# Optimization experiments

Measured on AMD Instinct MI355X. Metric: run time of the kernel, lower is better.

The kernel has to match this reference:

```python
import jax, jax.numpy as jnp
import numpy as np

EPS_DEFAULT = 1.1920928955078125e-07  # torch fp32 finfo eps used when eps=None


def rms_norm(x, ndims, weight=None, eps=EPS_DEFAULT):
    # normalize over the last `ndims` dims, matching F.rms_norm semantics
    axes = tuple(range(x.ndim - ndims, x.ndim))
    ms = jnp.mean(jnp.square(x), axis=axes, keepdims=True)
    out = x * jax.lax.rsqrt(ms + eps)
    if weight is not None:
        out = out * weight  # weight broadcasts over trailing dims
    return out


def setup_inputs() -> dict:
    key = jax.random.key(0)
    ks = jax.random.split(key, 9)
    B, S = 32, 512
    return {
        "x": jax.random.normal(ks[0], (B, S, 12, 24), dtype=jnp.float32),
        "y": jax.random.normal(ks[1], (B, S, 12, 16), dtype=jnp.float32),
        "z": jax.random.normal(ks[2], (B, S, 12, 16, 24), dtype=jnp.float32),
        "w0": jax.random.uniform(ks[3], (24,), dtype=jnp.float32),
        "w1": jax.random.uniform(ks[4], (12, 16), dtype=jnp.float32),
        "w2": jax.random.uniform(ks[5], (24,), dtype=jnp.float32),
        "w3": jax.random.uniform(ks[6], (24,), dtype=jnp.float32),
        "w4": jax.random.uniform(ks[7], (12, 16), dtype=jnp.float32),
        "w5": jax.random.uniform(ks[8], (24,), dtype=jnp.float32),
    }


def reference(x, y, z, w0, w1, w2, w3, w4, w5):
    # x branch: norm over (24,), then (12,24), then (24,)
    x = rms_norm(x, 1, w0)
    x = rms_norm(x, 2, None)
    x = rms_norm(x, 1, w3)
    # y branch: norm over (16,) eps=1e-3, then (12,16) twice
    y = rms_norm(y, 1, None, eps=0.001)
    y = rms_norm(y, 2, w1)
    y = rms_norm(y, 2, w4)
    # z branch: norm over (24,), then (12,16,24) eps=1e-2, then (24,)
    z = rms_norm(z, 1, w2)
    z = rms_norm(z, 3, None, eps=0.01)
    z = rms_norm(z, 1, w5)
    return (x, y, z)
```

## Files before the change

kernel.cpp:

```cpp
#include <hip/hip_runtime.h>

#define EPS_DEF 1.1920928955078125e-07f


__launch_bounds__(256)
__global__ void fused_rms_kernel(const float* __restrict__ x,
                                 const float* __restrict__ y,
                                 const float* __restrict__ z,
                                 const float* __restrict__ w0,
                                 const float* __restrict__ w1,
                                 const float* __restrict__ w2,
                                 const float* __restrict__ w3,
                                 const float* __restrict__ w4,
                                 const float* __restrict__ w5,
                                 float* __restrict__ ox,
                                 float* __restrict__ oy,
                                 float* __restrict__ oz)
{
    __shared__ float zs[192 * 25];
    __shared__ float xs[12 * 25];
    __shared__ float ys[12 * 17];
    __shared__ float w0s[24], w2s[24], w3s[24], w5s[24];
    __shared__ float w1s[192], w4s[192];
    __shared__ float wpart[4][4];
    __shared__ float az[192], ax[12], ay[12];

    const int tid = threadIdx.x;
    const int bid = blockIdx.x;

    if (tid < 24) {
        w0s[tid] = w0[tid];
        w2s[tid] = w2[tid];
        w3s[tid] = w3[tid];
        w5s[tid] = w5[tid];
    }
    if (tid < 192) {
        w1s[tid] = w1[tid];
        w4s[tid] = w4[tid];
    }

    const float4* zp = (const float4*)(z + (size_t)bid * 4608);
    const float4* xp = (const float4*)(x + (size_t)bid * 288);
    const float4* yp = (const float4*)(y + (size_t)bid * 192);

    for (int v = tid; v < 1152; v += 256) {
        float4 q = zp[v];
        int k = v * 4, r = k / 24, c = k - r * 24;
        float* d = &zs[r * 25 + c];
        d[0] = q.x; d[1] = q.y; d[2] = q.z; d[3] = q.w;
    }
    if (tid < 72) {
        float4 q = xp[tid];
        int k = tid * 4, r = k / 24, c = k - r * 24;
        float* d = &xs[r * 25 + c];
        d[0] = q.x; d[1] = q.y; d[2] = q.z; d[3] = q.w;
    }
    if (tid < 48) {
        float4 q = yp[tid];
        int k = tid * 4, r = k / 16, c = k - r * 16;
        float* d = &ys[r * 17 + c];
        d[0] = q.x; d[1] = q.y; d[2] = q.z; d[3] = q.w;
    }
    __syncthreads();

    float p0 = 0.f, p1 = 0.f, p2 = 0.f, p3 = 0.f;
    float r1 = 0.f, sw = 0.f;

    if (tid < 192) {
        const float* row = &zs[tid * 25];
        float s0 = 0.f, s = 0.f;
        #pragma unroll
        for (int j = 0; j < 24; ++j) {
            float v = row[j];
            float vw = v * w2s[j];
            s0 += v * v;
            s += vw * vw;
        }
        r1 = rsqrtf(s0 * (1.f / 24.f) + EPS_DEF);
        sw = s;
        p0 = r1 * r1 * s;
    } else if (tid < 204) {
        int i = tid - 192;
        const float* row = &xs[i * 25];
        float s0 = 0.f, s = 0.f;
        #pragma unroll
        for (int j = 0; j < 24; ++j) {
            float v = row[j];
            float vw = v * w0s[j];
            s0 += v * v;
            s += vw * vw;
        }
        r1 = rsqrtf(s0 * (1.f / 24.f) + EPS_DEF);
        sw = s;
        p1 = r1 * r1 * s;
    } else if (tid < 216) {
        int i = tid - 204;
        const float* row = &ys[i * 17];
        const float* w1r = &w1s[i * 16];
        float s0 = 0.f, s = 0.f;
        #pragma unroll
        for (int j = 0; j < 16; ++j) {
            float v = row[j];
            float vw = v * w1r[j];
            s0 += v * v;
            s += vw * vw;
        }
        r1 = rsqrtf(s0 * (1.f / 16.f) + 1e-3f);
        sw = s;
        p2 = r1 * r1 * s0;
        p3 = r1 * r1 * s;
    }

    #pragma unroll
    for (int d = 32; d > 0; d >>= 1) {
        p0 += __shfl_down(p0, d, 64);
        p1 += __shfl_down(p1, d, 64);
        p2 += __shfl_down(p2, d, 64);
        p3 += __shfl_down(p3, d, 64);
    }
    const int wave = tid >> 6;
    if ((tid & 63) == 0) {
        wpart[wave][0] = p0; wpart[wave][1] = p1;
        wpart[wave][2] = p2; wpart[wave][3] = p3;
    }
    __syncthreads();

    const float Sz  = wpart[0][0] + wpart[1][0] + wpart[2][0] + wpart[3][0];
    const float Sx  = wpart[0][1] + wpart[1][1] + wpart[2][1] + wpart[3][1];
    const float Sy0 = wpart[0][2] + wpart[1][2] + wpart[2][2] + wpart[3][2];
    const float Sy1 = wpart[0][3] + wpart[1][3] + wpart[2][3] + wpart[3][3];

    const float cZ  = rsqrtf(Sz  * (1.f / 4608.f) + 0.01f);
    const float cX  = rsqrtf(Sx  * (1.f / 288.f)  + EPS_DEF);
    const float c2y = rsqrtf(Sy0 * (1.f / 192.f)  + EPS_DEF);
    const float c3y = rsqrtf(c2y * c2y * Sy1 * (1.f / 192.f) + EPS_DEF);

    if (tid < 192) {
        float r3 = rsqrtf(cZ * cZ * r1 * r1 * sw * (1.f / 24.f) + EPS_DEF);
        az[tid] = r1 * cZ * r3;
    } else if (tid < 204) {
        float r3 = rsqrtf(cX * cX * r1 * r1 * sw * (1.f / 24.f) + EPS_DEF);
        ax[tid - 192] = r1 * cX * r3;
    } else if (tid < 216) {
        ay[tid - 204] = r1 * c2y * c3y;
    }
    __syncthreads();

    float4* ozp = (float4*)(oz + (size_t)bid * 4608);
    for (int v = tid; v < 1152; v += 256) {
        int k = v * 4, r = k / 24, c = k - r * 24;
        const float* s = &zs[r * 25 + c];
        float a = az[r];
        float4 q;
        q.x = s[0] * a * w2s[c + 0] * w5s[c + 0];
        q.y = s[1] * a * w2s[c + 1] * w5s[c + 1];
        q.z = s[2] * a * w2s[c + 2] * w5s[c + 2];
        q.w = s[3] * a * w2s[c + 3] * w5s[c + 3];
        ozp[v] = q;
    }
    if (tid < 72) {
        int k = tid * 4, r = k / 24, c = k - r * 24;
        const float* s = &xs[r * 25 + c];
        float a = ax[r];
        float4 q;
        q.x = s[0] * a * w0s[c + 0] * w3s[c + 0];
        q.y = s[1] * a * w0s[c + 1] * w3s[c + 1];
        q.z = s[2] * a * w0s[c + 2] * w3s[c + 2];
        q.w = s[3] * a * w0s[c + 3] * w3s[c + 3];
        ((float4*)(ox + (size_t)bid * 288))[tid] = q;
    }
    if (tid < 48) {
        int k = tid * 4, r = k / 16, c = k - r * 16;
        const float* s = &ys[r * 17 + c];
        float a = ay[r];
        float4 q;
        q.x = s[0] * a * w1s[k + 0] * w4s[k + 0];
        q.y = s[1] * a * w1s[k + 1] * w4s[k + 1];
        q.z = s[2] * a * w1s[k + 2] * w4s[k + 2];
        q.w = s[3] * a * w1s[k + 3] * w4s[k + 3];
        ((float4*)(oy + (size_t)bid * 192))[tid] = q;
    }
}

extern "C" void kernel_launch(void* const* d_in, const int* in_sizes, int n_in,
                              void* d_out, int out_size, void* d_ws, size_t ws_size,
                              hipStream_t stream) {
    const float* x  = (const float*)d_in[0];
    const float* y  = (const float*)d_in[1];
    const float* z  = (const float*)d_in[2];
    const float* w0 = (const float*)d_in[3];
    const float* w1 = (const float*)d_in[4];
    const float* w2 = (const float*)d_in[5];
    const float* w3 = (const float*)d_in[6];
    const float* w4 = (const float*)d_in[7];
    const float* w5 = (const float*)d_in[8];

    float* out = (float*)d_out;
    const size_t NX = (size_t)32 * 512 * 12 * 24;
    const size_t NY = (size_t)32 * 512 * 12 * 16;
    float* ox = out;
    float* oy = out + NX;
    float* oz = out + NX + NY;

    const int nblk = 32 * 512;
    hipLaunchKernelGGL(fused_rms_kernel, dim3(nblk), dim3(256), 0, stream,
                       x, y, z, w0, w1, w2, w3, w4, w5, ox, oy, oz);
}
```

Measured before the change: 139.1 us.

## Keep z rows in registers per thread and precompute squared and combined weights

Each of 192 threads now loads one 24-element z row straight into registers, so z no longer goes through LDS and the az broadcast array plus one barrier are dropped. The weights are precombined once per block into squared and product forms, which saves multiplies. Block size falls from 256 to 192, and x/y row outputs are written per row. In exchange, each thread's global accesses are strided by 96 bytes, so loads and stores are less coalesced per instruction, and register pressure rises from holding 24 floats.

```diff
diff --git a/kernel.cpp b/kernel.cpp
--- a/kernel.cpp
+++ b/kernel.cpp
@@ -3,7 +3,7 @@
 #define EPS_DEF 1.1920928955078125e-07f
 
 
-__launch_bounds__(256)
+__launch_bounds__(192)
 __global__ void fused_rms_kernel(const float* __restrict__ x,
                                  const float* __restrict__ y,
                                  const float* __restrict__ z,
@@ -17,168 +17,155 @@
                                  float* __restrict__ oy,
                                  float* __restrict__ oz)
 {
-    __shared__ float zs[192 * 25];
     __shared__ float xs[12 * 25];
     __shared__ float ys[12 * 17];
-    __shared__ float w0s[24], w2s[24], w3s[24], w5s[24];
-    __shared__ float w1s[192], w4s[192];
-    __shared__ float wpart[4][4];
-    __shared__ float az[192], ax[12], ay[12];
+    __shared__ float w2sqs[24], w25s[24];
+    __shared__ float w0sqs[24], w03s[24];
+    __shared__ float w1sqs[192], w14s[192];
+    __shared__ float wpart[3][4];
 
     const int tid = threadIdx.x;
     const int bid = blockIdx.x;
 
-    if (tid < 24) {
-        w0s[tid] = w0[tid];
-        w2s[tid] = w2[tid];
-        w3s[tid] = w3[tid];
-        w5s[tid] = w5[tid];
-    }
-    if (tid < 192) {
-        w1s[tid] = w1[tid];
-        w4s[tid] = w4[tid];
+    const float4* zp4 = (const float4*)(z + (size_t)bid * 4608 + tid * 24);
+    float zr[24];
+    #pragma unroll
+    for (int i = 0; i < 6; ++i) {
+        float4 q = zp4[i];
+        zr[4*i+0] = q.x; zr[4*i+1] = q.y; zr[4*i+2] = q.z; zr[4*i+3] = q.w;
     }
 
-    const float4* zp = (const float4*)(z + (size_t)bid * 4608);
-    const float4* xp = (const float4*)(x + (size_t)bid * 288);
-    const float4* yp = (const float4*)(y + (size_t)bid * 192);
-
-    for (int v = tid; v < 1152; v += 256) {
-        float4 q = zp[v];
-        int k = v * 4, r = k / 24, c = k - r * 24;
-        float* d = &zs[r * 25 + c];
-        d[0] = q.x; d[1] = q.y; d[2] = q.z; d[3] = q.w;
-    }
     if (tid < 72) {
-        float4 q = xp[tid];
+        float4 q = ((const float4*)(x + (size_t)bid * 288))[tid];
         int k = tid * 4, r = k / 24, c = k - r * 24;
         float* d = &xs[r * 25 + c];
         d[0] = q.x; d[1] = q.y; d[2] = q.z; d[3] = q.w;
-    }
-    if (tid < 48) {
-        float4 q = yp[tid];
-        int k = tid * 4, r = k / 16, c = k - r * 16;
+    } else if (tid < 120) {
+        int t = tid - 72;
+        float4 q = ((const float4*)(y + (size_t)bid * 192))[t];
+        int k = t * 4, r = k / 16, c = k - r * 16;
         float* d = &ys[r * 17 + c];
         d[0] = q.x; d[1] = q.y; d[2] = q.z; d[3] = q.w;
+    } else if (tid < 144) {
+        int j = tid - 120;
+        float a0 = w0[j], a2 = w2[j], a3 = w3[j], a5 = w5[j];
+        w0sqs[j] = a0 * a0; w03s[j] = a0 * a3;
+        w2sqs[j] = a2 * a2; w25s[j] = a2 * a5;
+    }
+    {
+        float a1 = w1[tid], a4 = w4[tid];
+        w1sqs[tid] = a1 * a1;
+        w14s[tid]  = a1 * a4;
     }
     __syncthreads();
 
-    float p0 = 0.f, p1 = 0.f, p2 = 0.f, p3 = 0.f;
-    float r1 = 0.f, sw = 0.f;
+    float s0 = 0.f, sw = 0.f;
+    #pragma unroll
+    for (int j = 0; j < 24; ++j) {
+        float v = zr[j];
+        s0 = fmaf(v, v, s0);
+        sw = fmaf(v * v, w2sqs[j], sw);
+    }
+    const float r1  = rsqrtf(s0 * (1.f / 24.f) + EPS_DEF);
+    const float r1sq = r1 * r1;
+    float p0 = r1sq * sw, p1 = 0.f, p2 = 0.f, p3 = 0.f;
 
-    if (tid < 192) {
-        const float* row = &zs[tid * 25];
-        float s0 = 0.f, s = 0.f;
+    float r1x = 0.f, swx = 0.f, r1y = 0.f;
+    if (tid < 12) {
+        const float* row = &xs[tid * 25];
+        float a0 = 0.f, aw = 0.f;
         #pragma unroll
         for (int j = 0; j < 24; ++j) {
             float v = row[j];
-            float vw = v * w2s[j];
-            s0 += v * v;
-            s += vw * vw;
+            a0 = fmaf(v, v, a0);
+            aw = fmaf(v * v, w0sqs[j], aw);
         }
-        r1 = rsqrtf(s0 * (1.f / 24.f) + EPS_DEF);
-        sw = s;
-        p0 = r1 * r1 * s;
-    } else if (tid < 204) {
-        int i = tid - 192;
-        const float* row = &xs[i * 25];
-        float s0 = 0.f, s = 0.f;
-        #pragma unroll
-        for (int j = 0; j < 24; ++j) {
-            float v = row[j];
-            float vw = v * w0s[j];
-            s0 += v * v;
-            s += vw * vw;
-        }
-        r1 = rsqrtf(s0 * (1.f / 24.f) + EPS_DEF);
-        sw = s;
-        p1 = r1 * r1 * s;
-    } else if (tid < 216) {
-        int i = tid - 204;
+        r1x = rsqrtf(a0 * (1.f / 24.f) + EPS_DEF);
+        swx = aw;
+        p1  = r1x * r1x * aw;
+    } else if (tid < 24) {
+        int i = tid - 12;
         const float* row = &ys[i * 17];
-        const float* w1r = &w1s[i * 16];
-        float s0 = 0.f, s = 0.f;
+        const float* wq  = &w1sqs[i * 16];
+        float a0 = 0.f, aw = 0.f;
         #pragma unroll
         for (int j = 0; j < 16; ++j) {
             float v = row[j];
-            float vw = v * w1r[j];
-            s0 += v * v;
-            s += vw * vw;
+            a0 = fmaf(v, v, a0);
+            aw = fmaf(v * v, wq[j], aw);
         }
-        r1 = rsqrtf(s0 * (1.f / 16.f) + 1e-3f);
-        sw = s;
-        p2 = r1 * r1 * s0;
-        p3 = r1 * r1 * s;
+        r1y = rsqrtf(a0 * (1.f / 16.f) + 1e-3f);
+        p2  = r1y * r1y * a0;
+        p3  = r1y * r1y * aw;
     }
 
     #pragma unroll
-    for (int d = 32; d > 0; d >>= 1) {
+    for (int d = 32; d; d >>= 1) {
         p0 += __shfl_down(p0, d, 64);
         p1 += __shfl_down(p1, d, 64);
         p2 += __shfl_down(p2, d, 64);
         p3 += __shfl_down(p3, d, 64);
     }
-    const int wave = tid >> 6;
     if ((tid & 63) == 0) {
-        wpart[wave][0] = p0; wpart[wave][1] = p1;
-        wpart[wave][2] = p2; wpart[wave][3] = p3;
+        int w = tid >> 6;
+        wpart[w][0] = p0; wpart[w][1] = p1; wpart[w][2] = p2; wpart[w][3] = p3;
     }
     __syncthreads();
 
-    const float Sz  = wpart[0][0] + wpart[1][0] + wpart[2][0] + wpart[3][0];
-    const float Sx  = wpart[0][1] + wpart[1][1] + wpart[2][1] + wpart[3][1];
-    const float Sy0 = wpart[0][2] + wpart[1][2] + wpart[2][2] + wpart[3][2];
-    const float Sy1 = wpart[0][3] + wpart[1][3] + wpart[2][3] + wpart[3][3];
+    const float Sz  = wpart[0][0] + wpart[1][0] + wpart[2][0];
+    const float Sx  = wpart[0][1] + wpart[1][1] + wpart[2][1];
+    const float Sy0 = wpart[0][2] + wpart[1][2] + wpart[2][2];
+    const float Sy1 = wpart[0][3] + wpart[1][3] + wpart[2][3];
 
     const float cZ  = rsqrtf(Sz  * (1.f / 4608.f) + 0.01f);
     const float cX  = rsqrtf(Sx  * (1.f / 288.f)  + EPS_DEF);
     const float c2y = rsqrtf(Sy0 * (1.f / 192.f)  + EPS_DEF);
     const float c3y = rsqrtf(c2y * c2y * Sy1 * (1.f / 192.f) + EPS_DEF);
 
-    if (tid < 192) {
-        float r3 = rsqrtf(cZ * cZ * r1 * r1 * sw * (1.f / 24.f) + EPS_DEF);
-        az[tid] = r1 * cZ * r3;
-    } else if (tid < 204) {
-        float r3 = rsqrtf(cX * cX * r1 * r1 * sw * (1.f / 24.f) + EPS_DEF);
-        ax[tid - 192] = r1 * cX * r3;
-    } else if (tid < 216) {
-        ay[tid - 204] = r1 * c2y * c3y;
+    {
+        float r3 = rsqrtf(cZ * cZ * r1sq * sw * (1.f / 24.f) + EPS_DEF);
+        float az = r1 * cZ * r3;
+        float4* op = (float4*)(oz + (size_t)bid * 4608 + tid * 24);
+        #pragma unroll
+        for (int i = 0; i < 6; ++i) {
+            float4 q;
+            q.x = zr[4*i+0] * az * w25s[4*i+0];
+            q.y = zr[4*i+1] * az * w25s[4*i+1];
+            q.z = zr[4*i+2] * az * w25s[4*i+2];
+            q.w = zr[4*i+3] * az * w25s[4*i+3];
+            op[i] = q;
+        }
     }
-    __syncthreads();
 
-    float4* ozp = (float4*)(oz + (size_t)bid * 4608);
-    for (int v = tid; v < 1152; v += 256) {
-        int k = v * 4, r = k / 24, c = k - r * 24;
-        const float* s = &zs[r * 25 + c];
-        float a = az[r];
-        float4 q;
-        q.x = s[0] * a * w2s[c + 0] * w5s[c + 0];
-        q.y = s[1] * a * w2s[c + 1] * w5s[c + 1];
-        q.z = s[2] * a * w2s[c + 2] * w5s[c + 2];
-        q.w = s[3] * a * w2s[c + 3] * w5s[c + 3];
-        ozp[v] = q;
-    }
-    if (tid < 72) {
-        int k = tid * 4, r = k / 24, c = k - r * 24;
-        const float* s = &xs[r * 25 + c];
-        float a = ax[r];
-        float4 q;
-        q.x = s[0] * a * w0s[c + 0] * w3s[c + 0];
-        q.y = s[1] * a * w0s[c + 1] * w3s[c + 1];
-        q.z = s[2] * a * w0s[c + 2] * w3s[c + 2];
-        q.w = s[3] * a * w0s[c + 3] * w3s[c + 3];
-        ((float4*)(ox + (size_t)bid * 288))[tid] = q;
-    }
-    if (tid < 48) {
-        int k = tid * 4, r = k / 16, c = k - r * 16;
-        const float* s = &ys[r * 17 + c];
-        float a = ay[r];
-        float4 q;
-        q.x = s[0] * a * w1s[k + 0] * w4s[k + 0];
-        q.y = s[1] * a * w1s[k + 1] * w4s[k + 1];
-        q.z = s[2] * a * w1s[k + 2] * w4s[k + 2];
-        q.w = s[3] * a * w1s[k + 3] * w4s[k + 3];
-        ((float4*)(oy + (size_t)bid * 192))[tid] = q;
+    if (tid < 12) {
+        float r3 = rsqrtf(cX * cX * r1x * r1x * swx * (1.f / 24.f) + EPS_DEF);
+        float ax = r1x * cX * r3;
+        const float* row = &xs[tid * 25];
+        float4* op = (float4*)(ox + (size_t)bid * 288 + tid * 24);
+        #pragma unroll
+        for (int i = 0; i < 6; ++i) {
+            float4 q;
+            q.x = row[4*i+0] * ax * w03s[4*i+0];
+            q.y = row[4*i+1] * ax * w03s[4*i+1];
+            q.z = row[4*i+2] * ax * w03s[4*i+2];
+            q.w = row[4*i+3] * ax * w03s[4*i+3];
+            op[i] = q;
+        }
+    } else if (tid < 24) {
+        int i = tid - 12;
+        float ay = r1y * c2y * c3y;
+        const float* row = &ys[i * 17];
+        const float* wf  = &w14s[i * 16];
+        float4* op = (float4*)(oy + (size_t)bid * 192 + i * 16);
+        #pragma unroll
+        for (int k = 0; k < 4; ++k) {
+            float4 q;
+            q.x = row[4*k+0] * ay * wf[4*k+0];
+            q.y = row[4*k+1] * ay * wf[4*k+1];
+            q.z = row[4*k+2] * ay * wf[4*k+2];
+            q.w = row[4*k+3] * ay * wf[4*k+3];
+            op[k] = q;
+        }
     }
 }
 
@@ -203,6 +190,6 @@
     float* oz = out + NX + NY;
 
     const int nblk = 32 * 512;
-    hipLaunchKernelGGL(fused_rms_kernel, dim3(nblk), dim3(256), 0, stream,
+    hipLaunchKernelGGL(fused_rms_kernel, dim3(nblk), dim3(192), 0, stream,
                        x, y, z, w0, w1, w2, w3, w4, w5, ox, oy, oz);
 }
```

New measurement: 174.0 us. 1.25x slower.
